# Performance work log

Measured on AMD Instinct MI355X. Metric: run time of the kernel, lower is better.

The kernel has to match this reference:

```python
import jax, jax.numpy as jnp
import numpy as np

B, S, H = 2, 1024, 2048
HEADS = 16
QC = 1536      # q_compressed_dim
KVC = 512      # kv_compressed_dim
ROPE = 64      # qk_rope_dim
NOPE = H // HEADS  # 128, non-rope head dim
VH = 128       # v_head_dim
INTER = 1408   # MoE intermediate dim
NSH = 2        # shared experts
NRT = 8        # routed experts
TOPK = 2
EPS = 1e-6


def setup_inputs() -> dict:
    key = jax.random.key(0)
    ks = jax.random.split(key, 16)

    def w(k, shape, scale=0.02):
        return jax.random.normal(k, shape, jnp.float32) * scale

    return {
        "x": jax.random.normal(ks[0], (B, S, H), jnp.float32),
        "freq": jax.random.uniform(ks[1], (S, ROPE // 2), jnp.float32, 0.0, 2.0 * np.pi),
        "mask": jnp.zeros((S, S), jnp.float32),
        "w_attn_norm": jnp.ones((H,), jnp.float32),
        "w_ffn_norm": jnp.ones((H,), jnp.float32),
        "W_dq": w(ks[2], (H, QC)),
        "q_c_norm": jnp.ones((QC,), jnp.float32),
        "W_uq": w(ks[3], (QC, HEADS * (NOPE + ROPE))),
        "W_dkv": w(ks[4], (H, KVC + ROPE)),
        "kv_c_norm": jnp.ones((KVC,), jnp.float32),
        "W_ukv": w(ks[5], (KVC, HEADS * (NOPE + VH))),
        "W_o": w(ks[6], (HEADS * VH, H)),
        "W_r": w(ks[7], (H, NRT)),
        "Ws_gate": w(ks[8], (NSH, H, INTER)),
        "Ws_up": w(ks[9], (NSH, H, INTER)),
        "Ws_down": w(ks[10], (NSH, INTER, H)),
        "We_gate": w(ks[11], (NRT, H, INTER)),
        "We_up": w(ks[12], (NRT, H, INTER)),
        "We_down": w(ks[13], (NRT, INTER, H)),
    }


def rmsnorm(x, w):
    return x * jax.lax.rsqrt(jnp.mean(x * x, axis=-1, keepdims=True) + EPS) * w


def rope_apply(x, cos, sin):
    # x: [..., S, D]; cos/sin: [S, D/2], interleaved-pair rotation
    x1 = x[..., 0::2]
    x2 = x[..., 1::2]
    return jnp.stack([x1 * cos - x2 * sin, x1 * sin + x2 * cos], axis=-1).reshape(x.shape)


def _experts(t, Wg, Wu, Wd):
    # t: [T,H]; W*: [E,H,I]/[E,I,H] -> [E,T,H], SwiGLU per expert
    hid = jax.nn.silu(jnp.einsum('th,ehi->eti', t, Wg)) * jnp.einsum('th,ehi->eti', t, Wu)
    return jnp.einsum('eti,eih->eth', hid, Wd)


def reference(x, freq, mask, w_attn_norm, w_ffn_norm, W_dq, q_c_norm, W_uq, W_dkv,
              kv_c_norm, W_ukv, W_o, W_r, Ws_gate, Ws_up, Ws_down,
              We_gate, We_up, We_down):
    Bb, Ss, Hh = x.shape
    cos = jnp.cos(freq)
    sin = jnp.sin(freq)

    # ---- MLA attention (pre-norm) ----
    h = rmsnorm(x, w_attn_norm)
    cq = rmsnorm(h @ W_dq, q_c_norm)                              # [B,S,QC]
    q = (cq @ W_uq).reshape(Bb, Ss, HEADS, NOPE + ROPE).transpose(0, 2, 1, 3)
    q_nope, q_rope = q[..., :NOPE], q[..., NOPE:]
    q_rope = rope_apply(q_rope, cos, sin)                          # [B,Hh,S,ROPE]

    ckv = h @ W_dkv                                               # [B,S,KVC+ROPE]
    kv_c = rmsnorm(ckv[..., :KVC], kv_c_norm)
    k_rope = rope_apply(ckv[..., KVC:], cos, sin)                  # [B,S,ROPE] shared over heads
    kv = (kv_c @ W_ukv).reshape(Bb, Ss, HEADS, NOPE + VH).transpose(0, 2, 1, 3)
    k_nope, v = kv[..., :NOPE], kv[..., NOPE:]

    scale = 1.0 / np.sqrt(NOPE + ROPE)
    scores = (jnp.einsum('bhsd,bhtd->bhst', q_nope, k_nope)
              + jnp.einsum('bhsd,btd->bhst', q_rope, k_rope)) * scale + mask
    attn = jax.nn.softmax(scores, axis=-1)
    attn_out = jnp.einsum('bhst,bhtd->bshd', attn, v).reshape(Bb, Ss, HEADS * VH) @ W_o
    x = x + attn_out

    # ---- DeepSeekMoE FFN (pre-norm) ----
    t = rmsnorm(x, w_ffn_norm).reshape(Bb * Ss, Hh)
    shared = _experts(t, Ws_gate, Ws_up, Ws_down).sum(axis=0)      # [T,H]
    probs = jax.nn.softmax(t @ W_r, axis=-1)                       # [T,E]
    vals, idx = jax.lax.top_k(probs, TOPK)
    weights = (jax.nn.one_hot(idx, NRT, dtype=t.dtype) * vals[..., None]).sum(axis=1)  # [T,E]
    routed = jnp.einsum('eth,te->th', _experts(t, We_gate, We_up, We_down), weights)
    return x + (shared + routed).reshape(Bb, Ss, Hh)
```

## Files before the change

### kernel.cpp

```cpp
#include <hip/hip_runtime.h>

typedef __bf16 bf16;
typedef _Float16 f16;
typedef unsigned short u16;
typedef __bf16 bf16x8 __attribute__((ext_vector_type(8)));
typedef _Float16 f16x8 __attribute__((ext_vector_type(8)));
typedef unsigned short u16x8 __attribute__((ext_vector_type(8)));
typedef float f32x4 __attribute__((ext_vector_type(4)));

#define TOK   2048
#define SEQ   1024
#define HIDD  2048
#define NHEADS 16
#define QCD   1536
#define KVCD  512
#define ROPED 64
#define NOPED 128
#define QDIM  192
#define VHD   128
#define KVD   576
#define KVDP  640
#define INTERD 1408
#define GUD   2816
#define RMS_EPS 1e-6f
#define SPS   64.0f
#define OSC   (1.0f/4096.0f)

__device__ inline void split64(float v, f16& h, f16& l) {
    v *= SPS; h = (f16)v; l = (f16)(v - (float)h);
}

__device__ inline void gl_lds16(const void* g, void* l) {
    __builtin_amdgcn_global_load_lds(
        (const __attribute__((address_space(1))) void*)g,
        (__attribute__((address_space(3))) void*)l,
        16, 0, 0);
}

#define WAITN(N) asm volatile("s_waitcnt vmcnt(" #N ")" ::: "memory")

__global__ __launch_bounds__(256) void tconv_ex3_kernel(const float* __restrict__ gate,
                                                        const float* __restrict__ up,
                                                        const float* __restrict__ down,
                                                        bf16* __restrict__ dGU,
                                                        bf16* __restrict__ dD) {
    const float* src; bf16* dst; int K, N, rowMul, rowAdd;
    if (blockIdx.z == 0)      { src = gate; dst = dGU; K = HIDD;   N = INTERD; rowMul = 2; rowAdd = 0; }
    else if (blockIdx.z == 1) { src = up;   dst = dGU; K = HIDD;   N = INTERD; rowMul = 2; rowAdd = 1; }
    else                      { src = down; dst = dD;  K = INTERD; N = HIDD;   rowMul = 1; rowAdd = 0; }
    int nb = blockIdx.x * 32, kb = blockIdx.y * 32;
    if (nb >= N || kb >= K) return;
    __shared__ float tile[32][33];
    int tx = threadIdx.x & 31, ty = threadIdx.x >> 5;
#pragma unroll
    for (int i = 0; i < 32; i += 8)
        tile[ty + i][tx] = src[(long)(kb + ty + i) * N + nb + tx];
    __syncthreads();
#pragma unroll
    for (int i = 0; i < 32; i += 8) {
        int n = nb + ty + i;
        dst[(long)(n * rowMul + rowAdd) * K + kb + tx] = (bf16)tile[tx][ty + i];
    }
}

__global__ __launch_bounds__(256) void tconv3h_kernel(const float* __restrict__ src,
                                                      f16* __restrict__ dst,
                                                      int K, int N, int Npad) {
    __shared__ float tile[32][33];
    int nb = blockIdx.x * 32, kb = blockIdx.y * 32;
    int tx = threadIdx.x & 31, ty = threadIdx.x >> 5;
#pragma unroll
    for (int i = 0; i < 32; i += 8) {
        int k = kb + ty + i, n = nb + tx;
        tile[ty + i][tx] = (k < K && n < N) ? src[(long)k * N + n] : 0.f;
    }
    __syncthreads();
#pragma unroll
    for (int i = 0; i < 32; i += 8) {
        int n = nb + ty + i, k = kb + tx;
        if (n < Npad && k < K) {
            f16 h, l; split64(tile[tx][ty + i], h, l);
            long base = (long)n * (3 * K) + k;
            dst[base] = h; dst[base + K] = l; dst[base + 2 * K] = h;
        }
    }
}

template<int F16, int TM, int TN>
__global__ __launch_bounds__(256) void gemm_bt_kernel(
    const u16* __restrict__ A, const u16* __restrict__ B, void* __restrict__ Cv,
    const float* __restrict__ aux, const int* __restrict__ idx,
    const int* __restrict__ cntPtr,
    int K, int lda, int ldb, int ldc,
    long sA, long sB, long sC,
    int mode, int auxLd, float osc)
{
    constexpr int AM = TM / 32;
    constexpr int AN = TN / 32;
    constexpr int NBUF = (TM + TN > 192) ? 2 : 3;
    constexpr int PF = NBUF - 1;
    constexpr int L = TM / 32 + TN / 32;
    __shared__ u16 As[NBUF][TM * 64];
    __shared__ u16 Bs[NBUF][TN * 64];
    const int bn = blockIdx.x, bm = blockIdx.y, z = blockIdx.z;
    int cnt = 1 << 30;
    if (cntPtr) {
        cnt = *cntPtr;
        int pad = (cnt + TM - 1) & ~(TM - 1);
        if (bm * TM >= pad) return;
    }
    const int tid = threadIdx.x, lane = tid & 63, w = tid >> 6;
    const int wm = w >> 1, wn = w & 1;
    const int lr = lane & 15;
    const int srow = lane >> 3, c16 = lane & 7;
    const u16* Ab = A + (long)z * sA + (long)bm * TM * lda;
    const u16* Bb = B + (long)z * sB + (long)bn * TN * ldb;
    f32x4 acc[AM][AN] = {};

    auto stage = [&](int buf, int k0) {
#pragma unroll
        for (int i = 0; i < TM / 32; i++) {
            int rb = i * 32 + w * 8;
            int row = rb + srow;
            int gc = ((c16 ^ (row & 7)) << 3);
            gl_lds16(&Ab[(long)row * lda + k0 + gc], &As[buf][rb * 64]);
        }
#pragma unroll
        for (int i = 0; i < TN / 32; i++) {
            int rb = i * 32 + w * 8;
            int row = rb + srow;
            int gc = ((c16 ^ (row & 7)) << 3);
            gl_lds16(&Bb[(long)row * ldb + k0 + gc], &Bs[buf][rb * 64]);
        }
    };
    auto compute = [&](int cur) {
#pragma unroll
        for (int ks = 0; ks < 2; ks++) {
            u16x8 af[AM], bfr[AN];
#pragma unroll
            for (int mi = 0; mi < AM; mi++) {
                int row = wm * (TM / 2) + mi * 16 + lr;
                int cg = (ks * 4 + (lane >> 4)) ^ (row & 7);
                af[mi] = *(const u16x8*)&As[cur][row * 64 + cg * 8];
            }
#pragma unroll
            for (int ni = 0; ni < AN; ni++) {
                int row = wn * (TN / 2) + ni * 16 + lr;
                int cg = (ks * 4 + (lane >> 4)) ^ (row & 7);
                bfr[ni] = *(const u16x8*)&Bs[cur][row * 64 + cg * 8];
            }
#pragma unroll
            for (int mi = 0; mi < AM; mi++)
#pragma unroll
                for (int ni = 0; ni < AN; ni++) {
                    if constexpr (F16)
                        acc[mi][ni] = __builtin_amdgcn_mfma_f32_16x16x32_f16(
                            __builtin_bit_cast(f16x8, af[mi]),
                            __builtin_bit_cast(f16x8, bfr[ni]), acc[mi][ni], 0, 0, 0);
                    else
                        acc[mi][ni] = __builtin_amdgcn_mfma_f32_16x16x32_bf16(
                            __builtin_bit_cast(bf16x8, af[mi]),
                            __builtin_bit_cast(bf16x8, bfr[ni]), acc[mi][ni], 0, 0, 0);
                }
        }
    };

    const int nk = K >> 6;
#pragma unroll
    for (int p = 0; p < PF; ++p) if (p < nk) stage(p, p << 6);

    if constexpr (PF == 2) {
        for (int t = 0; t < nk; ++t) {
            if (t + PF < nk) stage((t + PF) % NBUF, (t + PF) << 6);
            const int inflight = (nk - 1 - t < PF) ? (nk - 1 - t) : PF;
            if (inflight >= 2) {
                if constexpr (L == 4) WAITN(8); else WAITN(12);
            } else if (inflight == 1) {
                if constexpr (L == 4) WAITN(4); else WAITN(6);
            } else {
                WAITN(0);
            }
            __builtin_amdgcn_s_barrier();
            __builtin_amdgcn_sched_barrier(0);
            compute(t % NBUF);
            __builtin_amdgcn_s_barrier();
        }
    } else {
        for (int t = 0; t < nk; ++t) {
            if (t + 1 < nk) stage((t + 1) & 1, (t + 1) << 6);
            if (t + 1 < nk) WAITN(8);
            else            WAITN(0);
            __builtin_amdgcn_s_barrier();
            __builtin_amdgcn_sched_barrier(0);
            compute(t & 1);
            __builtin_amdgcn_s_barrier();
        }
    }

    const int r0 = (lane >> 4) << 2;
    const int rowBase = bm * TM + wm * (TM / 2);
    const int colBase = bn * TN + wn * (TN / 2);
#pragma unroll
    for (int mi = 0; mi < AM; mi++) {
#pragma unroll
        for (int ni = 0; ni < AN; ni++) {
#pragma unroll
            for (int r = 0; r < 4; r++) {
                int row = rowBase + mi * 16 + r0 + r;
                int col = colBase + ni * 16 + lr;
                float val = acc[mi][ni][r] * osc;
                long ci = (long)z * sC + (long)row * ldc + col;
                if (mode == 0) {
                    ((float*)Cv)[ci] = val;
                } else if (mode == 2) {
                    ((float*)Cv)[ci] = val + aux[(long)row * auxLd + col];
                } else if (mode == 3) {
                    float s = aux ? aux[(long)row * auxLd] : 1.f;
                    ((float*)Cv)[ci] += s * val;
                } else if (mode == 5) {
                    if (row < cnt) {
                        int tok = idx[row];
                        ((float*)Cv)[(long)tok * ldc + col] += aux[(long)tok * auxLd] * val;
                    }
                } else if (mode == 7) {
                    float other = __shfl_xor(val, 1, 64);
                    if (!(lane & 1)) {
                        float g = val, u = other;
                        ((bf16*)Cv)[(long)row * auxLd + (col >> 1)] =
                            (bf16)(g / (1.f + expf(-g)) * u);
                    }
                } else {
                    f16 h = (f16)val; f16 l = (f16)(val - (float)h);
                    ((f16*)Cv)[ci] = h; ((f16*)Cv)[ci + auxLd] = h; ((f16*)Cv)[ci + 2 * auxLd] = l;
                }
            }
        }
    }
}

__global__ __launch_bounds__(256) void rmsnorm_kernel(const float* __restrict__ in,
                                                      const float* __restrict__ w,
                                                      bf16* __restrict__ outB,
                                                      float* __restrict__ copyOut, int C) {
    long row = blockIdx.x;
    const float* r = in + row * C;
    float ss = 0.f;
    for (int i = threadIdx.x; i < C; i += 256) { float v = r[i]; ss += v * v; }
    for (int off = 32; off > 0; off >>= 1) ss += __shfl_down(ss, off, 64);
    __shared__ float red[5];
    int lane = threadIdx.x & 63, wv = threadIdx.x >> 6;
    if (lane == 0) red[wv] = ss;
    __syncthreads();
    if (threadIdx.x == 0) red[4] = rsqrtf((red[0] + red[1] + red[2] + red[3]) / C + RMS_EPS);
    __syncthreads();
    float sc = red[4];
    for (int i = threadIdx.x; i < C; i += 256) {
        outB[row * C + i] = (bf16)(r[i] * sc * w[i]);
        if (copyOut) copyOut[row * C + i] = r[i];
    }
}

__global__ __launch_bounds__(256) void rmsnorm3h_kernel(const float* __restrict__ in,
                                                        const float* __restrict__ w,
                                                        f16* __restrict__ out3, int C) {
    long row = blockIdx.x;
    const float* r = in + row * C;
    float ss = 0.f;
    for (int i = threadIdx.x; i < C; i += 256) { float v = r[i]; ss += v * v; }
    for (int off = 32; off > 0; off >>= 1) ss += __shfl_down(ss, off, 64);
    __shared__ float red[5];
    int lane = threadIdx.x & 63, wv = threadIdx.x >> 6;
    if (lane == 0) red[wv] = ss;
    __syncthreads();
    if (threadIdx.x == 0) red[4] = rsqrtf((red[0] + red[1] + red[2] + red[3]) / C + RMS_EPS);
    __syncthreads();
    float sc = red[4];
    f16* o = out3 + row * (3L * C);
    for (int i = threadIdx.x; i < C; i += 256) {
        f16 h, l; split64(r[i] * sc * w[i], h, l);
        o[i] = h; o[C + i] = h; o[2 * C + i] = l;
    }
}

__global__ __launch_bounds__(256) void kvsplit3h_kernel(const float* __restrict__ ckv,
                                                        const float* __restrict__ nrm,
                                                        const float* __restrict__ freq,
                                                        f16* __restrict__ kvc3,
                                                        float* __restrict__ krope) {
    int t = blockIdx.x; int s = t & (SEQ - 1);
    const float* r = ckv + (long)t * KVDP;
    float ss = 0.f;
    for (int i = threadIdx.x; i < KVCD; i += 256) { float v = r[i]; ss += v * v; }
    for (int off = 32; off > 0; off >>= 1) ss += __shfl_down(ss, off, 64);
    __shared__ float red[5];
    int lane = threadIdx.x & 63, wv = threadIdx.x >> 6;
    if (lane == 0) red[wv] = ss;
    __syncthreads();
    if (threadIdx.x == 0) red[4] = rsqrtf((red[0] + red[1] + red[2] + red[3]) / KVCD + RMS_EPS);
    __syncthreads();
    float sc = red[4];
    f16* o = kvc3 + (long)t * (3 * KVCD);
    for (int i = threadIdx.x; i < KVCD; i += 256) {
        f16 h, l; split64(r[i] * sc * nrm[i], h, l);
        o[i] = h; o[KVCD + i] = h; o[2 * KVCD + i] = l;
    }
    if (threadIdx.x < 32) {
        int i = threadIdx.x;
        float f = freq[s * 32 + i], c = cosf(f), sn = sinf(f);
        float x1 = r[KVCD + 2 * i], x2 = r[KVCD + 2 * i + 1];
        krope[(long)t * ROPED + 2 * i]     = x1 * c - x2 * sn;
        krope[(long)t * ROPED + 2 * i + 1] = x1 * sn + x2 * c;
    }
}

__global__ __launch_bounds__(256) void build_q3h_kernel(const float* __restrict__ qpre,
                                                        const float* __restrict__ freq,
                                                        f16* __restrict__ q3) {
    int t = blockIdx.x; int b = t >> 10, s = t & (SEQ - 1);
    for (int idx = threadIdx.x; idx < NHEADS * 96; idx += 256) {
        int h = idx / 96, j = idx % 96;
        const float* qrow = qpre + (long)t * 3072 + h * QDIM;
        f16* dst = q3 + ((long)(b * NHEADS + h) * SEQ + s) * (3 * QDIM);
        if (j < 64) {
            int d = 2 * j;
#pragma unroll
            for (int u = 0; u < 2; u++) {
                f16 hh, ll; split64(qrow[d + u], hh, ll);
                dst[d + u] = hh; dst[QDIM + d + u] = hh; dst[2 * QDIM + d + u] = ll;
            }
        } else {
            int i = j - 64;
            float f = freq[s * 32 + i], c = cosf(f), sn = sinf(f);
            float x1 = qrow[NOPED + 2 * i], x2 = qrow[NOPED + 2 * i + 1];
            float v0 = x1 * c - x2 * sn, v1 = x1 * sn + x2 * c;
            int d = NOPED + 2 * i;
            f16 h0, l0, h1, l1; split64(v0, h0, l0); split64(v1, h1, l1);
            dst[d] = h0; dst[QDIM + d] = h0; dst[2 * QDIM + d] = l0;
            dst[d + 1] = h1; dst[QDIM + d + 1] = h1; dst[2 * QDIM + d + 1] = l1;
        }
    }
}

__global__ __launch_bounds__(256) void build_k3h_kernel(const float* __restrict__ kv,
                                                        const float* __restrict__ krope,
                                                        f16* __restrict__ k3,
                                                        f16* __restrict__ v3T) {
    int t = blockIdx.x; int b = t >> 10, s = t & (SEQ - 1);
    const float* kvrow = kv + (long)t * 4096;
    const float* kr = krope + (long)t * ROPED;
    for (int idx = threadIdx.x; idx < NHEADS * 96; idx += 256) {
        int h = idx / 96, j = idx % 96;
        f16* dst = k3 + ((long)(b * NHEADS + h) * SEQ + s) * (3 * QDIM);
        float v0, v1; int d;
        if (j < 64) { d = 2 * j; v0 = kvrow[h * 256 + d]; v1 = kvrow[h * 256 + d + 1]; }
        else { int i = j - 64; d = NOPED + 2 * i; v0 = kr[2 * i]; v1 = kr[2 * i + 1]; }
        f16 h0, l0, h1, l1; split64(v0, h0, l0); split64(v1, h1, l1);
        dst[d] = h0; dst[QDIM + d] = l0; dst[2 * QDIM + d] = h0;
        dst[d + 1] = h1; dst[QDIM + d + 1] = l1; dst[2 * QDIM + d + 1] = h1;
    }
    for (int idx = threadIdx.x; idx < NHEADS * VHD; idx += 256) {
        int h = idx >> 7, d = idx & 127;
        f16 hh, ll; split64(kvrow[h * 256 + NOPED + d], hh, ll);
        long base = ((long)(b * NHEADS + h) * VHD + d) * (3 * SEQ) + s;
        v3T[base] = hh; v3T[base + SEQ] = ll; v3T[base + 2 * SEQ] = hh;
    }
}

__global__ __launch_bounds__(256) void softmax3h_kernel(const float* __restrict__ scores,
                                                        const float* __restrict__ mask,
                                                        f16* __restrict__ P3, float scale) {
    int s = blockIdx.x, h = blockIdx.y;
    const float* row  = scores + ((long)h * SEQ + s) * SEQ;
    const float* mrow = mask + (long)s * SEQ;
    f16* prow = P3 + ((long)h * SEQ + s) * (3 * SEQ);
    float v[4]; float m = -1e30f;
#pragma unroll
    for (int j = 0; j < 4; j++) {
        int i = threadIdx.x + j * 256;
        v[j] = row[i] * scale + mrow[i];
        m = fmaxf(m, v[j]);
    }
    for (int off = 32; off > 0; off >>= 1) m = fmaxf(m, __shfl_down(m, off, 64));
    __shared__ float redm[5], reds[5];
    int lane = threadIdx.x & 63, wv = threadIdx.x >> 6;
    if (lane == 0) redm[wv] = m;
    __syncthreads();
    if (threadIdx.x == 0) redm[4] = fmaxf(fmaxf(redm[0], redm[1]), fmaxf(redm[2], redm[3]));
    __syncthreads();
    float M = redm[4];
    float sum = 0.f;
#pragma unroll
    for (int j = 0; j < 4; j++) { v[j] = expf(v[j] - M); sum += v[j]; }
    for (int off = 32; off > 0; off >>= 1) sum += __shfl_down(sum, off, 64);
    if (lane == 0) reds[wv] = sum;
    __syncthreads();
    if (threadIdx.x == 0) reds[4] = reds[0] + reds[1] + reds[2] + reds[3];
    __syncthreads();
    float inv = 1.f / reds[4];
#pragma unroll
    for (int j = 0; j < 4; j++) {
        int i = threadIdx.x + j * 256;
        f16 hh, ll; split64(v[j] * inv, hh, ll);
        prow[i] = hh; prow[SEQ + i] = hh; prow[2 * SEQ + i] = ll;
    }
}

__global__ void zero_counts_kernel(int* counts) {
    if (threadIdx.x < 8) counts[threadIdx.x] = 0;
}

__global__ __launch_bounds__(64) void router_kernel(const float* __restrict__ x2,
                                                    const float* __restrict__ wffn,
                                                    const float* __restrict__ Wr,
                                                    float* __restrict__ wts,
                                                    int* __restrict__ perm,
                                                    int* __restrict__ counts) {
    int t = blockIdx.x; int lane = threadIdx.x;
    const float* r = x2 + (long)t * HIDD;
    float ss = 0.f;
    for (int k = lane; k < HIDD; k += 64) { float v = r[k]; ss += v * v; }
    for (int off = 32; off > 0; off >>= 1) ss += __shfl_down(ss, off, 64);
    float sc = rsqrtf(__shfl(ss, 0, 64) / HIDD + RMS_EPS);
    float acc[8] = {0, 0, 0, 0, 0, 0, 0, 0};
    for (int k = lane; k < HIDD; k += 64) {
        float tv = r[k] * sc * wffn[k];
        const float* wr = Wr + (long)k * 8;
#pragma unroll
        for (int e = 0; e < 8; e++) acc[e] += tv * wr[e];
    }
#pragma unroll
    for (int e = 0; e < 8; e++)
        for (int off = 32; off > 0; off >>= 1) acc[e] += __shfl_down(acc[e], off, 64);
    if (lane == 0) {
        float m = acc[0];
#pragma unroll
        for (int e = 1; e < 8; e++) m = fmaxf(m, acc[e]);
        float p[8]; float se = 0.f;
#pragma unroll
        for (int e = 0; e < 8; e++) { p[e] = expf(acc[e] - m); se += p[e]; }
        float inv = 1.f / se;
        int i1 = 0; float v1 = p[0];
        for (int e = 1; e < 8; e++) if (p[e] > v1) { v1 = p[e]; i1 = e; }
        int i2 = -1; float v2 = -1.f;
        for (int e = 0; e < 8; e++) if (e != i1 && p[e] > v2) { v2 = p[e]; i2 = e; }
#pragma unroll
        for (int e = 0; e < 8; e++)
            wts[(long)t * 8 + e] = (e == i1) ? v1 * inv : ((e == i2) ? v2 * inv : 0.f);
        int s1 = atomicAdd(&counts[i1], 1); perm[i1 * TOK + s1] = t;
        int s2 = atomicAdd(&counts[i2], 1); perm[i2 * TOK + s2] = t;
    }
}

__global__ __launch_bounds__(256) void gather8_kernel(const bf16* __restrict__ tbuf,
                                                      const int* __restrict__ perm,
                                                      const int* __restrict__ counts,
                                                      bf16* __restrict__ tA8) {
    int e = blockIdx.y, row = blockIdx.x;
    int cnt = counts[e];
    int pad = (cnt + 127) & ~127;
    if (row >= pad) return;
    bf16* tA = tA8 + (size_t)e * TOK * HIDD;
    int i = threadIdx.x * 8;
    if (row < cnt) {
        int tok = perm[e * TOK + row];
        *(bf16x8*)&tA[(long)row * HIDD + i] = *(const bf16x8*)&tbuf[(long)tok * HIDD + i];
    } else {
        bf16x8 z = {};
        *(bf16x8*)&tA[(long)row * HIDD + i] = z;
    }
}

static inline size_t alignup(size_t v) { return (v + 255) & ~(size_t)255; }

extern "C" void kernel_launch(void* const* d_in, const int* in_sizes, int n_in,
                              void* d_out, int out_size, void* d_ws, size_t ws_size,
                              hipStream_t stream) {
    const float* x       = (const float*)d_in[0];
    const float* freq    = (const float*)d_in[1];
    const float* mask    = (const float*)d_in[2];
    const float* w_attn  = (const float*)d_in[3];
    const float* w_ffn   = (const float*)d_in[4];
    const float* W_dq    = (const float*)d_in[5];
    const float* q_c_nrm = (const float*)d_in[6];
    const float* W_uq    = (const float*)d_in[7];
    const float* W_dkv   = (const float*)d_in[8];
    const float* kv_nrm  = (const float*)d_in[9];
    const float* W_ukv   = (const float*)d_in[10];
    const float* W_o     = (const float*)d_in[11];
    const float* W_r     = (const float*)d_in[12];
    const float* Ws_gate = (const float*)d_in[13];
    const float* Ws_up   = (const float*)d_in[14];
    const float* Ws_down = (const float*)d_in[15];
    const float* We_gate = (const float*)d_in[16];
    const float* We_up   = (const float*)d_in[17];
    const float* We_down = (const float*)d_in[18];
    float* out = (float*)d_out;
    char* ws = (char*)d_ws;
    (void)in_sizes; (void)n_in; (void)out_size;

    size_t o = 0;
    auto alloc = [&](size_t n) { size_t r = o; o += alignup(n); return r; };
    size_t oWslot = alloc((size_t)3072 * 3 * QCD * 2);
    size_t oQ3    = alloc((size_t)32 * SEQ * 3 * QDIM * 2);
    size_t oK3    = alloc((size_t)32 * SEQ * 3 * QDIM * 2);
    size_t oV3T   = alloc((size_t)32 * VHD * 3 * SEQ * 2);
    size_t oAttn3 = alloc((size_t)TOK * 3 * HIDD * 2);
    size_t oX2    = alloc((size_t)TOK * HIDD * 4);
    size_t oTbuf  = alloc((size_t)TOK * HIDD * 2);
    size_t oWts   = alloc((size_t)TOK * 8 * 4);
    size_t oPerm  = alloc((size_t)8 * TOK * 4);
    size_t oCnt   = alloc((size_t)8 * 4);
    size_t oKrope = alloc((size_t)TOK * ROPED * 4);
    size_t zH3   = alignup((size_t)TOK * 3 * HIDD * 2);
    size_t zCqp  = alignup((size_t)TOK * QCD * 4);
    size_t zCq3  = alignup((size_t)TOK * 3 * QCD * 2);
    size_t zQp   = alignup((size_t)TOK * 3072 * 4);
    size_t zCkv  = alignup((size_t)TOK * KVDP * 4);
    size_t zKvc3 = alignup((size_t)TOK * 3 * KVCD * 2);
    size_t zKv   = alignup((size_t)TOK * 4096 * 4);
    size_t chain = zH3 + zCqp + zCq3 + zQp + zCkv + zKvc3 + zKv;
    size_t zScores = alignup((size_t)16 * SEQ * SEQ * 4);
    size_t zP3     = alignup((size_t)16 * SEQ * 3 * SEQ * 2);
    size_t zTA8    = alignup((size_t)8 * TOK * HIDD * 2);
    size_t zHid    = alignup((size_t)TOK * INTERD * 2);
    size_t arenaSz = chain;
    if (zScores + zP3 > arenaSz) arenaSz = zScores + zP3;
    if (zTA8 + zHid > arenaSz) arenaSz = zTA8 + zHid;
    size_t oArena = alloc(arenaSz);
    if (ws_size < o) return;

    size_t oH3   = oArena;
    size_t oCqp  = oH3 + zH3;
    size_t oCq3  = oCqp + zCqp;
    size_t oQp   = oCq3 + zCq3;
    size_t oCkv  = oQp + zQp;
    size_t oKvc3 = oCkv + zCkv;
    size_t oKv   = oKvc3 + zKvc3;
    size_t oScores = oArena;
    size_t oP3     = oArena + zScores;
    size_t oTA8    = oArena;
    size_t oHid    = oArena + zTA8;

    f16*  wslotH = (f16*)(ws + oWslot);
    bf16* wslotB = (bf16*)(ws + oWslot);
    bf16* wslotB2 = (bf16*)(ws + oWslot + (size_t)GUD * HIDD * 2);
    f16*  q3    = (f16*)(ws + oQ3);
    f16*  k3    = (f16*)(ws + oK3);
    f16*  v3T   = (f16*)(ws + oV3T);
    f16*  attn3 = (f16*)(ws + oAttn3);
    float* x2   = (float*)(ws + oX2);
    bf16* tbuf  = (bf16*)(ws + oTbuf);
    float* wts  = (float*)(ws + oWts);
    int*  perm  = (int*)(ws + oPerm);
    int*  counts = (int*)(ws + oCnt);
    float* krope = (float*)(ws + oKrope);
    f16*  h3    = (f16*)(ws + oH3);
    float* cqpre = (float*)(ws + oCqp);
    f16*  cq3   = (f16*)(ws + oCq3);
    float* qpre = (float*)(ws + oQp);
    float* ckv  = (float*)(ws + oCkv);
    f16*  kvc3  = (f16*)(ws + oKvc3);
    float* kv   = (float*)(ws + oKv);
    float* scores = (float*)(ws + oScores);
    f16*  P3    = (f16*)(ws + oP3);
    bf16* tA8   = (bf16*)(ws + oTA8);
    bf16* hid   = (bf16*)(ws + oHid);

    auto tconv3h = [&](const float* src, f16* dst, int K, int N, int Npad) {
        dim3 g((Npad + 31) / 32, (K + 31) / 32);
        tconv3h_kernel<<<g, 256, 0, stream>>>(src, dst, K, N, Npad);
    };
    auto tconvEx = [&](const float* gate, const float* up, const float* down) {
        tconv_ex3_kernel<<<dim3(64, 64, 3), 256, 0, stream>>>(gate, up, down, wslotB, wslotB2);
    };
    auto gH128x128 = [&](const f16* A, const f16* B, void* C, const float* aux,
                         int M, int N, int K, int lda, int ldb, int ldc,
                         long sA, long sB, long sC, int Z, int mode, int auxLd, float osc) {
        dim3 g(N / 128, M / 128, Z);
        gemm_bt_kernel<1, 128, 128><<<g, 256, 0, stream>>>((const u16*)A, (const u16*)B, C, aux,
            nullptr, nullptr, K, lda, ldb, ldc, sA, sB, sC, mode, auxLd, osc);
    };
    auto gH128x64 = [&](const f16* A, const f16* B, void* C, const float* aux,
                        int M, int N, int K, int lda, int ldb, int ldc,
                        long sA, long sB, long sC, int Z, int mode, int auxLd, float osc) {
        dim3 g(N / 64, M / 128, Z);
        gemm_bt_kernel<1, 128, 64><<<g, 256, 0, stream>>>((const u16*)A, (const u16*)B, C, aux,
            nullptr, nullptr, K, lda, ldb, ldc, sA, sB, sC, mode, auxLd, osc);
    };
    auto gH64x64 = [&](const f16* A, const f16* B, void* C, const float* aux,
                       int M, int N, int K, int lda, int ldb, int ldc,
                       long sA, long sB, long sC, int Z, int mode, int auxLd, float osc) {
        dim3 g(N / 64, M / 64, Z);
        gemm_bt_kernel<1, 64, 64><<<g, 256, 0, stream>>>((const u16*)A, (const u16*)B, C, aux,
            nullptr, nullptr, K, lda, ldb, ldc, sA, sB, sC, mode, auxLd, osc);
    };
    auto gB128x64 = [&](const bf16* A, const bf16* B, void* C,
                        const float* aux, const int* idx, const int* cnt,
                        int M, int N, int K, int lda, int ldb, int ldc, int mode, int auxLd) {
        dim3 g(N / 64, M / 128, 1);
        gemm_bt_kernel<0, 128, 64><<<g, 256, 0, stream>>>((const u16*)A, (const u16*)B, C, aux,
            idx, cnt, K, lda, ldb, ldc, 0, 0, 0, mode, auxLd, 1.0f);
    };
    auto gB64x64 = [&](const bf16* A, const bf16* B, void* C,
                       const float* aux, const int* idx, const int* cnt,
                       int M, int N, int K, int lda, int ldb, int ldc, int mode, int auxLd) {
        dim3 g(N / 64, M / 64, 1);
        gemm_bt_kernel<0, 64, 64><<<g, 256, 0, stream>>>((const u16*)A, (const u16*)B, C, aux,
            idx, cnt, K, lda, ldb, ldc, 0, 0, 0, mode, auxLd, 1.0f);
    };

    rmsnorm3h_kernel<<<TOK, 256, 0, stream>>>(x, w_attn, h3, HIDD);

    tconv3h(W_dq, wslotH, HIDD, QCD, QCD);
    gH128x64(h3, wslotH, cqpre, nullptr, TOK, QCD, 3 * HIDD, 3 * HIDD, 3 * HIDD, QCD,
             0, 0, 0, 1, 0, 0, OSC);
    rmsnorm3h_kernel<<<TOK, 256, 0, stream>>>(cqpre, q_c_nrm, cq3, QCD);

    tconv3h(W_uq, wslotH, QCD, 3072, 3072);
    gH128x128(cq3, wslotH, qpre, nullptr, TOK, 3072, 3 * QCD, 3 * QCD, 3 * QCD, 3072,
              0, 0, 0, 1, 0, 0, OSC);

    tconv3h(W_dkv, wslotH, HIDD, KVD, KVDP);
    gH64x64(h3, wslotH, ckv, nullptr, TOK, KVDP, 3 * HIDD, 3 * HIDD, 3 * HIDD, KVDP,
            0, 0, 0, 1, 0, 0, OSC);
    kvsplit3h_kernel<<<TOK, 256, 0, stream>>>(ckv, kv_nrm, freq, kvc3, krope);

    tconv3h(W_ukv, wslotH, KVCD, 4096, 4096);
    gH128x128(kvc3, wslotH, kv, nullptr, TOK, 4096, 3 * KVCD, 3 * KVCD, 3 * KVCD, 4096,
              0, 0, 0, 1, 0, 0, OSC);

    build_q3h_kernel<<<TOK, 256, 0, stream>>>(qpre, freq, q3);
    build_k3h_kernel<<<TOK, 256, 0, stream>>>(kv, krope, k3, v3T);

    for (int b = 0; b < 2; b++) {
        int h0 = b * NHEADS;
        gH128x128(q3 + (size_t)h0 * SEQ * 3 * QDIM, k3 + (size_t)h0 * SEQ * 3 * QDIM,
                  scores, nullptr, SEQ, SEQ, 3 * QDIM, 3 * QDIM, 3 * QDIM, SEQ,
                  (long)SEQ * 3 * QDIM, (long)SEQ * 3 * QDIM, (long)SEQ * SEQ, 16, 0, 0, OSC);
        softmax3h_kernel<<<dim3(SEQ, 16), 256, 0, stream>>>(scores, mask, P3,
                                                            1.f / sqrtf((float)QDIM));
        gH64x64(P3, v3T + (size_t)h0 * VHD * 3 * SEQ,
                attn3 + (size_t)b * SEQ * 3 * HIDD, nullptr,
                SEQ, VHD, 3 * SEQ, 3 * SEQ, 3 * SEQ, 3 * HIDD,
                (long)SEQ * 3 * SEQ, (long)VHD * 3 * SEQ, (long)VHD, 16, 6, HIDD,
                1.0f / SPS);
    }

    tconv3h(W_o, wslotH, HIDD, HIDD, HIDD);
    gH128x64(attn3, wslotH, x2, x, TOK, HIDD, 3 * HIDD, 3 * HIDD, 3 * HIDD, HIDD,
             0, 0, 0, 1, 2, HIDD, OSC);

    rmsnorm_kernel<<<TOK, 256, 0, stream>>>(x2, w_ffn, tbuf, out, HIDD);
    zero_counts_kernel<<<1, 64, 0, stream>>>(counts);
    router_kernel<<<TOK, 64, 0, stream>>>(x2, w_ffn, W_r, wts, perm, counts);
    gather8_kernel<<<dim3(TOK, 8), 256, 0, stream>>>(tbuf, perm, counts, tA8);

    for (int e = 0; e < 2; e++) {
        tconvEx(Ws_gate + (size_t)e * HIDD * INTERD,
                Ws_up   + (size_t)e * HIDD * INTERD,
                Ws_down + (size_t)e * INTERD * HIDD);
        gB128x64(tbuf, wslotB, hid, nullptr, nullptr, nullptr,
                 TOK, GUD, HIDD, HIDD, HIDD, GUD, 7, INTERD);
        gB128x64(hid, wslotB2, out, nullptr, nullptr, nullptr,
                 TOK, HIDD, INTERD, INTERD, INTERD, HIDD, 3, 0);
    }
    for (int e = 0; e < 8; e++) {
        tconvEx(We_gate + (size_t)e * HIDD * INTERD,
                We_up   + (size_t)e * HIDD * INTERD,
                We_down + (size_t)e * INTERD * HIDD);
        gB64x64(tA8 + (size_t)e * TOK * HIDD, wslotB, hid, nullptr, nullptr, counts + e,
                TOK, GUD, HIDD, HIDD, HIDD, GUD, 7, INTERD);
        gB64x64(hid, wslotB2, out, wts + e, perm + (size_t)e * TOK, counts + e,
                TOK, HIDD, INTERD, INTERD, INTERD, HIDD, 5, 8);
    }
}
```

Measured before the change: 1.612 ms.

## Batch routed experts into grouped GEMMs with fused gather and atomic scatter

Replaces the per-expert loop of eight weight conversions and sixteen small GEMM launches with two batched weight-conversion kernels and two grouped GEMMs that use blockIdx.z as the expert index. The separate gather kernel is removed: the gate/up GEMM loads activation rows directly through the permutation index. The down GEMM scatters into the output with atomicAdd, since experts now run concurrently and can hit the same token. The intent is to cut launch overhead and fill the GPU with all experts at once. The cost is much larger workspace for all expert weights and hidden activations, plus atomic contention and non-deterministic summation order.

```diff
diff --git a/kernel.cpp b/kernel.cpp
--- a/kernel.cpp
+++ b/kernel.cpp
@@ -61,6 +61,43 @@
         int n = nb + ty + i;
         dst[(long)(n * rowMul + rowAdd) * K + kb + tx] = (bf16)tile[tx][ty + i];
     }
+}
+
+__global__ __launch_bounds__(256) void tconv_guall_kernel(const float* __restrict__ gate,
+                                                          const float* __restrict__ up,
+                                                          bf16* __restrict__ dstAll) {
+    int e = blockIdx.z >> 1, isUp = blockIdx.z & 1;
+    const float* src = (isUp ? up : gate) + (size_t)e * HIDD * INTERD;
+    bf16* dst = dstAll + (size_t)e * GUD * HIDD;
+    int nb = blockIdx.x * 32, kb = blockIdx.y * 32;
+    __shared__ float tile[32][33];
+    int tx = threadIdx.x & 31, ty = threadIdx.x >> 5;
+#pragma unroll
+    for (int i = 0; i < 32; i += 8)
+        tile[ty + i][tx] = src[(long)(kb + ty + i) * INTERD + nb + tx];
+    __syncthreads();
+#pragma unroll
+    for (int i = 0; i < 32; i += 8) {
+        int n = nb + ty + i;
+        dst[(long)(n * 2 + isUp) * HIDD + kb + tx] = (bf16)tile[tx][ty + i];
+    }
+}
+
+__global__ __launch_bounds__(256) void tconv_downall_kernel(const float* __restrict__ down,
+                                                            bf16* __restrict__ dstAll) {
+    int e = blockIdx.z;
+    const float* src = down + (size_t)e * INTERD * HIDD;
+    bf16* dst = dstAll + (size_t)e * HIDD * INTERD;
+    int nb = blockIdx.x * 32, kb = blockIdx.y * 32;
+    __shared__ float tile[32][33];
+    int tx = threadIdx.x & 31, ty = threadIdx.x >> 5;
+#pragma unroll
+    for (int i = 0; i < 32; i += 8)
+        tile[ty + i][tx] = src[(long)(kb + ty + i) * HIDD + nb + tx];
+    __syncthreads();
+#pragma unroll
+    for (int i = 0; i < 32; i += 8)
+        dst[(long)(nb + ty + i) * INTERD + kb + tx] = (bf16)tile[tx][ty + i];
 }
 
 __global__ __launch_bounds__(256) void tconv3h_kernel(const float* __restrict__ src,
@@ -105,7 +142,7 @@
     const int bn = blockIdx.x, bm = blockIdx.y, z = blockIdx.z;
     int cnt = 1 << 30;
     if (cntPtr) {
-        cnt = *cntPtr;
+        cnt = cntPtr[z];
         int pad = (cnt + TM - 1) & ~(TM - 1);
         if (bm * TM >= pad) return;
     }
@@ -117,13 +154,26 @@
     const u16* Bb = B + (long)z * sB + (long)bn * TN * ldb;
     f32x4 acc[AM][AN] = {};
 
+    const bool aidx = (idx != nullptr && mode == 7);
+    int iperm[4];
+    if (aidx) {
+#pragma unroll
+        for (int i = 0; i < TM / 32; i++) {
+            int r = bm * TM + i * 32 + w * 8 + srow;
+            int v = idx[(long)z * TOK + r];
+            iperm[i] = (r < cnt) ? v : 0;
+        }
+    }
+
     auto stage = [&](int buf, int k0) {
 #pragma unroll
         for (int i = 0; i < TM / 32; i++) {
             int rb = i * 32 + w * 8;
             int row = rb + srow;
             int gc = ((c16 ^ (row & 7)) << 3);
-            gl_lds16(&Ab[(long)row * lda + k0 + gc], &As[buf][rb * 64]);
+            const u16* src = aidx ? (A + (long)iperm[i] * lda + k0 + gc)
+                                  : (Ab + (long)row * lda + k0 + gc);
+            gl_lds16(src, &As[buf][rb * 64]);
         }
 #pragma unroll
         for (int i = 0; i < TN / 32; i++) {
@@ -219,14 +269,15 @@
                     ((float*)Cv)[ci] += s * val;
                 } else if (mode == 5) {
                     if (row < cnt) {
-                        int tok = idx[row];
-                        ((float*)Cv)[(long)tok * ldc + col] += aux[(long)tok * auxLd] * val;
+                        int tok = idx[(long)z * TOK + row];
+                        atomicAdd(&((float*)Cv)[(long)tok * ldc + col],
+                                  aux[(long)tok * auxLd + z] * val);
                     }
                 } else if (mode == 7) {
                     float other = __shfl_xor(val, 1, 64);
                     if (!(lane & 1)) {
                         float g = val, u = other;
-                        ((bf16*)Cv)[(long)row * auxLd + (col >> 1)] =
+                        ((bf16*)Cv)[(long)z * sC + (long)row * auxLd + (col >> 1)] =
                             (bf16)(g / (1.f + expf(-g)) * u);
                     }
                 } else {
@@ -448,25 +499,6 @@
             wts[(long)t * 8 + e] = (e == i1) ? v1 * inv : ((e == i2) ? v2 * inv : 0.f);
         int s1 = atomicAdd(&counts[i1], 1); perm[i1 * TOK + s1] = t;
         int s2 = atomicAdd(&counts[i2], 1); perm[i2 * TOK + s2] = t;
-    }
-}
-
-__global__ __launch_bounds__(256) void gather8_kernel(const bf16* __restrict__ tbuf,
-                                                      const int* __restrict__ perm,
-                                                      const int* __restrict__ counts,
-                                                      bf16* __restrict__ tA8) {
-    int e = blockIdx.y, row = blockIdx.x;
-    int cnt = counts[e];
-    int pad = (cnt + 127) & ~127;
-    if (row >= pad) return;
-    bf16* tA = tA8 + (size_t)e * TOK * HIDD;
-    int i = threadIdx.x * 8;
-    if (row < cnt) {
-        int tok = perm[e * TOK + row];
-        *(bf16x8*)&tA[(long)row * HIDD + i] = *(const bf16x8*)&tbuf[(long)tok * HIDD + i];
-    } else {
-        bf16x8 z = {};
-        *(bf16x8*)&tA[(long)row * HIDD + i] = z;
     }
 }
 
@@ -521,11 +553,11 @@
     size_t chain = zH3 + zCqp + zCq3 + zQp + zCkv + zKvc3 + zKv;
     size_t zScores = alignup((size_t)16 * SEQ * SEQ * 4);
     size_t zP3     = alignup((size_t)16 * SEQ * 3 * SEQ * 2);
-    size_t zTA8    = alignup((size_t)8 * TOK * HIDD * 2);
-    size_t zHid    = alignup((size_t)TOK * INTERD * 2);
+    size_t zHid8   = alignup((size_t)8 * TOK * INTERD * 2);
+    size_t zWegu   = alignup((size_t)8 * GUD * HIDD * 2);
     size_t arenaSz = chain;
     if (zScores + zP3 > arenaSz) arenaSz = zScores + zP3;
-    if (zTA8 + zHid > arenaSz) arenaSz = zTA8 + zHid;
+    if (zHid8 + zWegu > arenaSz) arenaSz = zHid8 + zWegu;
     size_t oArena = alloc(arenaSz);
     if (ws_size < o) return;
 
@@ -538,8 +570,8 @@
     size_t oKv   = oKvc3 + zKvc3;
     size_t oScores = oArena;
     size_t oP3     = oArena + zScores;
-    size_t oTA8    = oArena;
-    size_t oHid    = oArena + zTA8;
+    size_t oHid8   = oArena;
+    size_t oWegu   = oArena + zHid8;
 
     f16*  wslotH = (f16*)(ws + oWslot);
     bf16* wslotB = (bf16*)(ws + oWslot);
@@ -563,8 +595,9 @@
     float* kv   = (float*)(ws + oKv);
     float* scores = (float*)(ws + oScores);
     f16*  P3    = (f16*)(ws + oP3);
-    bf16* tA8   = (bf16*)(ws + oTA8);
-    bf16* hid   = (bf16*)(ws + oHid);
+    bf16* hid8  = (bf16*)(ws + oHid8);
+    bf16* WeguAll = (bf16*)(ws + oWegu);
+    bf16* WedAll  = (bf16*)(ws + oWegu);
 
     auto tconv3h = [&](const float* src, f16* dst, int K, int N, int Npad) {
         dim3 g((Npad + 31) / 32, (K + 31) / 32);
@@ -601,13 +634,6 @@
         gemm_bt_kernel<0, 128, 64><<<g, 256, 0, stream>>>((const u16*)A, (const u16*)B, C, aux,
             idx, cnt, K, lda, ldb, ldc, 0, 0, 0, mode, auxLd, 1.0f);
     };
-    auto gB64x64 = [&](const bf16* A, const bf16* B, void* C,
-                       const float* aux, const int* idx, const int* cnt,
-                       int M, int N, int K, int lda, int ldb, int ldc, int mode, int auxLd) {
-        dim3 g(N / 64, M / 64, 1);
-        gemm_bt_kernel<0, 64, 64><<<g, 256, 0, stream>>>((const u16*)A, (const u16*)B, C, aux,
-            idx, cnt, K, lda, ldb, ldc, 0, 0, 0, mode, auxLd, 1.0f);
-    };
 
     rmsnorm3h_kernel<<<TOK, 256, 0, stream>>>(x, w_attn, h3, HIDD);
 
@@ -653,24 +679,32 @@
     rmsnorm_kernel<<<TOK, 256, 0, stream>>>(x2, w_ffn, tbuf, out, HIDD);
     zero_counts_kernel<<<1, 64, 0, stream>>>(counts);
     router_kernel<<<TOK, 64, 0, stream>>>(x2, w_ffn, W_r, wts, perm, counts);
-    gather8_kernel<<<dim3(TOK, 8), 256, 0, stream>>>(tbuf, perm, counts, tA8);
 
     for (int e = 0; e < 2; e++) {
         tconvEx(Ws_gate + (size_t)e * HIDD * INTERD,
                 Ws_up   + (size_t)e * HIDD * INTERD,
                 Ws_down + (size_t)e * INTERD * HIDD);
-        gB128x64(tbuf, wslotB, hid, nullptr, nullptr, nullptr,
+        gB128x64(tbuf, wslotB, hid8, nullptr, nullptr, nullptr,
                  TOK, GUD, HIDD, HIDD, HIDD, GUD, 7, INTERD);
-        gB128x64(hid, wslotB2, out, nullptr, nullptr, nullptr,
+        gB128x64(hid8, wslotB2, out, nullptr, nullptr, nullptr,
                  TOK, HIDD, INTERD, INTERD, INTERD, HIDD, 3, 0);
     }
-    for (int e = 0; e < 8; e++) {
-        tconvEx(We_gate + (size_t)e * HIDD * INTERD,
-                We_up   + (size_t)e * HIDD * INTERD,
-                We_down + (size_t)e * INTERD * HIDD);
-        gB64x64(tA8 + (size_t)e * TOK * HIDD, wslotB, hid, nullptr, nullptr, counts + e,
-                TOK, GUD, HIDD, HIDD, HIDD, GUD, 7, INTERD);
-        gB64x64(hid, wslotB2, out, wts + e, perm + (size_t)e * TOK, counts + e,
-                TOK, HIDD, INTERD, INTERD, INTERD, HIDD, 5, 8);
-    }
-}
+
+    tconv_guall_kernel<<<dim3(INTERD / 32, HIDD / 32, 16), 256, 0, stream>>>(
+        We_gate, We_up, WeguAll);
+    {
+        dim3 g(GUD / 64, TOK / 64, 8);
+        gemm_bt_kernel<0, 64, 64><<<g, 256, 0, stream>>>(
+            (const u16*)tbuf, (const u16*)WeguAll, hid8, nullptr, perm, counts,
+            HIDD, HIDD, HIDD, 0, 0, (long)GUD * HIDD, (long)TOK * INTERD, 7, INTERD, 1.0f);
+    }
+    tconv_downall_kernel<<<dim3(HIDD / 32, INTERD / 32, 8), 256, 0, stream>>>(
+        We_down, WedAll);
+    {
+        dim3 g(HIDD / 64, TOK / 64, 8);
+        gemm_bt_kernel<0, 64, 64><<<g, 256, 0, stream>>>(
+            (const u16*)hid8, (const u16*)WedAll, out, wts, perm, counts,
+            INTERD, INTERD, INTERD, HIDD, (long)TOK * INTERD, (long)HIDD * INTERD, 0,
+            5, 8, 1.0f);
+    }
+}
```

Measured after the change: 1.390 ms. 13.8% less time.
